# Optimization experiments

Hardware: AMD Instinct MI355X
Metric: run time of the kernel (lower is better)

Reference implementation:

```python
import jax, jax.numpy as jnp
from jax import lax
import numpy as np

B, S_DEC, S_ENC = 32, 128, 128
V, E, H = 32000, 200, 128


def setup_inputs() -> dict:
    key = jax.random.key(0)
    ks = jax.random.split(key, 10)
    emb = jax.random.normal(ks[0], (V, E), dtype=jnp.float32)
    emb = emb.at[0].set(0.0)  # padding_idx row (char2id[' '] -> 0)
    return {
        "sequence": jax.random.randint(ks[1], (B, S_DEC), 0, V),
        "hs": jax.random.normal(ks[2], (B, S_ENC, H), dtype=jnp.float32),
        "h": jax.random.normal(ks[3], (1, B, H), dtype=jnp.float32),
        "emb": emb,
        "w_ih": jax.random.normal(ks[4], (3 * H, E), dtype=jnp.float32) * 0.05,
        "w_hh": jax.random.normal(ks[5], (3 * H, H), dtype=jnp.float32) * 0.05,
        "b_ih": jax.random.normal(ks[6], (3 * H,), dtype=jnp.float32) * 0.05,
        "b_hh": jax.random.normal(ks[7], (3 * H,), dtype=jnp.float32) * 0.05,
        "w_out": jax.random.normal(ks[8], (V, 2 * H), dtype=jnp.float32) * 0.05,
        "b_out": jax.random.normal(ks[9], (V,), dtype=jnp.float32) * 0.05,
    }


def _gru(x_gates, h0, w_hh, b_hh):
    # x_gates: [B, S, 3H] precomputed input projections; torch gate order r,z,n
    def step(hprev, xg):
        hg = hprev @ w_hh.T + b_hh
        xr, xz, xn = jnp.split(xg, 3, axis=-1)
        hr, hz, hn = jnp.split(hg, 3, axis=-1)
        r = jax.nn.sigmoid(xr + hr)
        z = jax.nn.sigmoid(xz + hz)
        n = jnp.tanh(xn + r * hn)
        hnew = (1.0 - z) * n + z * hprev
        return hnew, hnew

    hT, outs = lax.scan(step, h0, jnp.swapaxes(x_gates, 0, 1))  # scan over time
    return jnp.swapaxes(outs, 0, 1), hT  # [B,S,H], [B,H]


def reference(sequence, hs, h, emb, w_ih, w_hh, b_ih, b_hh, w_out, b_out):
    # Embedding lookup (padding row already zero)
    x = emb[sequence]  # [B, S_dec, E]
    x_gates = jnp.einsum("bse,ge->bsg", x, w_ih) + b_ih  # [B, S_dec, 3H]
    output, hT = _gru(x_gates, h[0], w_hh, b_hh)  # [B, S_dec, H]
    state = hT[None]  # [1, B, H]
    # s = bmm(hs, output^T): [B, S_enc, S_dec]; softmax over encoder axis (dim=1)
    s = jnp.einsum("beh,bdh->bed", hs, output)
    attention_weight = jax.nn.softmax(s, axis=1)
    # context: replaces the per-timestep python loop with one contraction
    c = jnp.einsum("bed,beh->bdh", attention_weight, hs)  # [B, S_dec, H]
    cat = jnp.concatenate([output, c], axis=-1)  # [B, S_dec, 2H]
    logits = jnp.einsum("bdh,vh->bdv", cat, w_out) + b_out  # [B, S_dec, V]
    return logits, state, attention_weight
```

## Files before the change

### kernel.cpp

```cpp
#include <hip/hip_runtime.h>
#include <hip/hip_bf16.h>

#define B_    32
#define SDEC  128
#define SENC  128
#define V_    32000
#define E_    200
#define H_    128
#define G3    384

typedef __attribute__((ext_vector_type(8))) short bf16x8;
typedef __attribute__((ext_vector_type(4))) float f32x4;

#define GLOBAL_AS __attribute__((address_space(1)))
#define LDS_AS    __attribute__((address_space(3)))

__device__ __forceinline__ float fast_sigmoid(float x) {
  return 1.f / (1.f + __expf(-x));
}
__device__ __forceinline__ float fast_tanh(float x) {
  float e2 = __expf(2.f * x);
  return 1.f - 2.f / (e2 + 1.f);
}

__global__ __launch_bounds__(192) void k_embed_proj(
    const int* __restrict__ seq, const float* __restrict__ emb,
    const float* __restrict__ w_ih, const float* __restrict__ b_ih,
    float* __restrict__ xg) {
  __shared__ __align__(16) float xs[16][E_];
  __shared__ int sidx[16];
  const int r0 = blockIdx.x * 16;
  const int t = threadIdx.x;
  if (t < 16) sidx[t] = seq[r0 + t];
  __syncthreads();
  for (int i = t; i < 800; i += 192) {
    int r = i / 50, c = i - r * 50;
    *(float4*)&xs[r][c * 4] =
        *(const float4*)(emb + (size_t)sidx[r] * E_ + c * 4);
  }
  __syncthreads();
  const int g0 = t, g1 = t + 192;
  float a0[16], a1[16];
#pragma unroll
  for (int r = 0; r < 16; r++) { a0[r] = 0.f; a1[r] = 0.f; }
  const float* w0 = w_ih + (size_t)g0 * E_;
  const float* w1 = w_ih + (size_t)g1 * E_;
  for (int k = 0; k < E_; k += 4) {
    float4 wv0 = *(const float4*)(w0 + k);
    float4 wv1 = *(const float4*)(w1 + k);
#pragma unroll
    for (int r = 0; r < 16; r++) {
      float4 xv = *(const float4*)&xs[r][k];
      a0[r] += wv0.x * xv.x + wv0.y * xv.y + wv0.z * xv.z + wv0.w * xv.w;
      a1[r] += wv1.x * xv.x + wv1.y * xv.y + wv1.z * xv.z + wv1.w * xv.w;
    }
  }
  const float b0 = b_ih[g0], b1 = b_ih[g1];
#pragma unroll
  for (int r = 0; r < 16; r++) {
    xg[(size_t)(r0 + r) * G3 + g0] = a0[r] + b0;
    xg[(size_t)(r0 + r) * G3 + g1] = a1[r] + b1;
  }
}

__global__ __launch_bounds__(512) void k_gru_cvt(
    const float* __restrict__ xg, const float* __restrict__ h0,
    const float* __restrict__ w_hh, const float* __restrict__ b_hh,
    float* __restrict__ cat, __hip_bfloat16* __restrict__ cat_bf,
    float* __restrict__ state_out,
    const float* __restrict__ w_out, __hip_bfloat16* __restrict__ wout_bf) {
  if (blockIdx.x >= 32) {
    int idx = ((blockIdx.x - 32) * 512 + threadIdx.x) * 8;
    float4 a = *(const float4*)(w_out + idx);
    float4 c = *(const float4*)(w_out + idx + 4);
    union { __hip_bfloat16 h[8]; uint4 v; } p;
    p.h[0] = __float2bfloat16(a.x); p.h[1] = __float2bfloat16(a.y);
    p.h[2] = __float2bfloat16(a.z); p.h[3] = __float2bfloat16(a.w);
    p.h[4] = __float2bfloat16(c.x); p.h[5] = __float2bfloat16(c.y);
    p.h[6] = __float2bfloat16(c.z); p.h[7] = __float2bfloat16(c.w);
    *(uint4*)(wout_bf + idx) = p.v;
    return;
  }

  const int b = blockIdx.x;
  const int t = threadIdx.x;
  const int hh = t >> 2;
  const int sub = t & 3;

  float wr_[32], wz_[32], wn_[32];
#pragma unroll
  for (int m = 0; m < 8; m++) {
    int c = (m + sub * 2) & 7;
    int kb = sub * 32 + c * 4;
    *(float4*)&wr_[m * 4] = *(const float4*)(w_hh + (size_t)hh * H_ + kb);
    *(float4*)&wz_[m * 4] = *(const float4*)(w_hh + (size_t)(128 + hh) * H_ + kb);
    *(float4*)&wn_[m * 4] = *(const float4*)(w_hh + (size_t)(256 + hh) * H_ + kb);
  }

  __shared__ __align__(16) float hp[2][H_];
  const float* xgb = xg + (size_t)b * SDEC * G3;
  const float br = b_hh[hh], bz = b_hh[128 + hh], bn = b_hh[256 + hh];
  float cxr = xgb[hh], cxz = xgb[128 + hh], cxn = xgb[256 + hh];
  if (t < H_) hp[0][t] = h0[b * H_ + t];
  float* catb = cat + (size_t)b * SDEC * 256;
  __hip_bfloat16* catbfb = cat_bf + (size_t)b * SDEC * 256;
  __syncthreads();

  int cur = 0;
  for (int s = 0; s < SDEC; s++) {
    float nxr = 0.f, nxz = 0.f, nxn = 0.f;
    if (s + 1 < SDEC) {
      const float* xp = xgb + (size_t)(s + 1) * G3;
      nxr = xp[hh]; nxz = xp[128 + hh]; nxn = xp[256 + hh];
    }
    float sr = 0.f, sz = 0.f, sn = 0.f;
#pragma unroll
    for (int m = 0; m < 8; m++) {
      int c = (m + sub * 2) & 7;
      float4 hv = *(const float4*)&hp[cur][sub * 32 + c * 4];
      sr += wr_[m * 4 + 0] * hv.x + wr_[m * 4 + 1] * hv.y +
            wr_[m * 4 + 2] * hv.z + wr_[m * 4 + 3] * hv.w;
      sz += wz_[m * 4 + 0] * hv.x + wz_[m * 4 + 1] * hv.y +
            wz_[m * 4 + 2] * hv.z + wz_[m * 4 + 3] * hv.w;
      sn += wn_[m * 4 + 0] * hv.x + wn_[m * 4 + 1] * hv.y +
            wn_[m * 4 + 2] * hv.z + wn_[m * 4 + 3] * hv.w;
    }
    sr += __shfl_xor(sr, 1); sr += __shfl_xor(sr, 2);
    sz += __shfl_xor(sz, 1); sz += __shfl_xor(sz, 2);
    sn += __shfl_xor(sn, 1); sn += __shfl_xor(sn, 2);

    float hold = hp[cur][hh];
    float r = fast_sigmoid(cxr + sr + br);
    float z = fast_sigmoid(cxz + sz + bz);
    float n = fast_tanh(cxn + r * (sn + bn));
    float hnew = (1.f - z) * n + z * hold;
    if (sub == 0) {
      hp[cur ^ 1][hh] = hnew;
      catb[(size_t)s * 256 + hh] = hnew;
      catbfb[(size_t)s * 256 + hh] = __float2bfloat16(hnew);
    }
    __syncthreads();
    cur ^= 1;
    cxr = nxr; cxz = nxz; cxn = nxn;
  }
  if (t < H_) state_out[b * H_ + t] = hp[cur][t];
}

__global__ __launch_bounds__(256) void k_attn(
    const float* __restrict__ hs, const float* __restrict__ cat,
    float* __restrict__ attw_out, __hip_bfloat16* __restrict__ cat_bf) {
  __shared__ __align__(16) float hsb[SENC][H_];
  __shared__ __align__(16) float ctb[64][H_];
  __shared__ __align__(16) float sbuf[64][SENC];
  const int b = blockIdx.x >> 1;
  const int d0 = (blockIdx.x & 1) * 64;
  const int t = threadIdx.x;
  const float* hsbase = hs + (size_t)b * SENC * H_;

  for (int i = t; i < 4096; i += 256) {
    int r = i >> 5, c4 = i & 31;
    int pc = c4 ^ ((r >> 3) & 3);
    *(f32x4*)&hsb[r][pc * 4] = *(const f32x4*)(hsbase + r * H_ + c4 * 4);
  }
  for (int i = t; i < 2048; i += 256) {
    int r = i >> 5, c4 = i & 31;
    int pc = c4 ^ ((r >> 2) & 7);
    *(f32x4*)&ctb[r][pc * 4] =
        *(const f32x4*)(cat + (size_t)(b * SDEC + d0 + r) * 256 + c4 * 4);
  }
  __syncthreads();

  {
    const int te = t >> 4, td = t & 15;
    const int sa = te & 3, sb2 = td & 7;
    float acc[8][4] = {};
    for (int k4 = 0; k4 < 32; k4++) {
      const int pa = (k4 ^ sa) * 4, pb = (k4 ^ sb2) * 4;
      f32x4 av[8], bv[4];
#pragma unroll
      for (int i = 0; i < 8; i++) av[i] = *(const f32x4*)&hsb[te * 8 + i][pa];
#pragma unroll
      for (int j = 0; j < 4; j++) bv[j] = *(const f32x4*)&ctb[td * 4 + j][pb];
#pragma unroll
      for (int i = 0; i < 8; i++)
#pragma unroll
        for (int j = 0; j < 4; j++)
          acc[i][j] += av[i][0] * bv[j][0] + av[i][1] * bv[j][1] +
                       av[i][2] * bv[j][2] + av[i][3] * bv[j][3];
    }
    const int swd = td & 7;
#pragma unroll
    for (int j = 0; j < 4; j++) {
      int drow = td * 4 + j;
      f32x4 v0 = {acc[0][j], acc[1][j], acc[2][j], acc[3][j]};
      f32x4 v1 = {acc[4][j], acc[5][j], acc[6][j], acc[7][j]};
      *(f32x4*)&sbuf[drow][((te * 2) ^ swd) * 4] = v0;
      *(f32x4*)&sbuf[drow][((te * 2 + 1) ^ swd) * 4] = v1;
    }
  }
  __syncthreads();

  {
    const int d = t >> 2, p = t & 3;
    const int swz = (d >> 2) & 7;
    f32x4 vals[8];
    float mx = -1e30f;
#pragma unroll
    for (int mm = 0; mm < 8; mm++) {
      int pc = p * 8 + mm;
      f32x4 v = *(const f32x4*)&sbuf[d][pc * 4];
      vals[mm] = v;
      mx = fmaxf(mx, fmaxf(fmaxf(v[0], v[1]), fmaxf(v[2], v[3])));
    }
    mx = fmaxf(mx, __shfl_xor(mx, 1));
    mx = fmaxf(mx, __shfl_xor(mx, 2));
    float sum = 0.f;
#pragma unroll
    for (int mm = 0; mm < 8; mm++) {
      f32x4 v = vals[mm];
      v[0] = __expf(v[0] - mx); v[1] = __expf(v[1] - mx);
      v[2] = __expf(v[2] - mx); v[3] = __expf(v[3] - mx);
      vals[mm] = v;
      sum += v[0] + v[1] + v[2] + v[3];
    }
    sum += __shfl_xor(sum, 1); sum += __shfl_xor(sum, 2);
    const float inv = 1.f / sum;
    float* aw = attw_out + (size_t)b * SENC * SDEC + d0 + d;
#pragma unroll
    for (int mm = 0; mm < 8; mm++) {
      int pc = p * 8 + mm;
      f32x4 v = vals[mm];
      v[0] *= inv; v[1] *= inv; v[2] *= inv; v[3] *= inv;
      *(f32x4*)&sbuf[d][pc * 4] = v;
      int c4 = pc ^ swz;
#pragma unroll
      for (int u = 0; u < 4; u++)
        aw[(size_t)(c4 * 4 + u) * SDEC] = v[u];
    }
  }
  __syncthreads();

  {
    const int td = t >> 4, th = t & 15;
    const int swd = td & 7;
    float acc[4][8] = {};
    for (int e4 = 0; e4 < 32; e4++) {
      const int pp = (e4 ^ swd) * 4;
      f32x4 pv[4];
#pragma unroll
      for (int i = 0; i < 4; i++) pv[i] = *(const f32x4*)&sbuf[td * 4 + i][pp];
#pragma unroll
      for (int j = 0; j < 4; j++) {
        int e = e4 * 4 + j;
        int sw = (e >> 3) & 3;
        f32x4 h0v = *(const f32x4*)&hsb[e][((th * 2) ^ sw) * 4];
        f32x4 h1v = *(const f32x4*)&hsb[e][((th * 2 + 1) ^ sw) * 4];
#pragma unroll
        for (int i = 0; i < 4; i++) {
          float pw = pv[i][j];
          acc[i][0] += pw * h0v[0]; acc[i][1] += pw * h0v[1];
          acc[i][2] += pw * h0v[2]; acc[i][3] += pw * h0v[3];
          acc[i][4] += pw * h1v[0]; acc[i][5] += pw * h1v[1];
          acc[i][6] += pw * h1v[2]; acc[i][7] += pw * h1v[3];
        }
      }
    }
#pragma unroll
    for (int i = 0; i < 4; i++) {
      union { __hip_bfloat16 hv[8]; uint4 v; } pk;
#pragma unroll
      for (int u = 0; u < 8; u++) pk.hv[u] = __float2bfloat16(acc[i][u]);
      *(uint4*)(cat_bf + (size_t)(b * SDEC + d0 + td * 4 + i) * 256 + 128 +
                th * 8) = pk.v;
    }
  }
}

__global__ __launch_bounds__(512) void k_gemm_mfma(
    const __hip_bfloat16* __restrict__ A, const __hip_bfloat16* __restrict__ Bw,
    const float* __restrict__ b_out, float* __restrict__ C) {
  constexpr int K = 256, N = V_, Kt = 32;
  alignas(16) __shared__ char smem[73728];
  __hip_bfloat16 (*As)[4096] = (__hip_bfloat16(*)[4096])smem;
  __hip_bfloat16 (*Bs)[8192] = (__hip_bfloat16(*)[8192])(smem + 24576);
  float* tr = (float*)smem;

  const int tid = threadIdx.x;
  const int w = tid >> 6, l = tid & 63;
  const int wr = w >> 2, wc = w & 3;
  const int lr = l & 15, lk = l >> 4;
  const int lq = l >> 2, lc = l & 3;

  const int bid = blockIdx.x;
  const int wgid = (bid & 7) * 500 + (bid >> 3);
  const int mt = wgid & 31;
  const int nt = wgid >> 5;
  const int m0 = mt * 128, n0 = nt * 256;

  f32x4 acc[4][4];
#pragma unroll
  for (int m = 0; m < 4; m++)
#pragma unroll
    for (int n = 0; n < 4; n++) acc[m][n] = (f32x4){0.f, 0.f, 0.f, 0.f};

#define STAGE(buf, kk)                                                            \
  do {                                                                            \
    const __hip_bfloat16* gA = A + (size_t)(m0 + w * 16 + lq) * K + (kk) + lc * 8;\
    const __hip_bfloat16* gB0 = Bw + (size_t)(n0 + w * 32 + lq) * K + (kk) + lc * 8;\
    const __hip_bfloat16* gB1 = gB0 + (size_t)16 * K;                             \
    __builtin_amdgcn_global_load_lds((const GLOBAL_AS void*)gA,                   \
        (LDS_AS void*)(&As[buf][w * 512]), 16, 0, 0);                             \
    __builtin_amdgcn_global_load_lds((const GLOBAL_AS void*)gB0,                  \
        (LDS_AS void*)(&Bs[buf][w * 1024]), 16, 0, 0);                            \
    __builtin_amdgcn_global_load_lds((const GLOBAL_AS void*)gB1,                  \
        (LDS_AS void*)(&Bs[buf][w * 1024 + 512]), 16, 0, 0);                      \
  } while (0)

  STAGE(0, 0);
  STAGE(1, Kt);

#pragma unroll
  for (int t = 0; t < 8; ++t) {
    if (t < 7) asm volatile("s_waitcnt vmcnt(3)" ::: "memory");
    else       asm volatile("s_waitcnt vmcnt(0)" ::: "memory");
    __builtin_amdgcn_s_barrier();
    asm volatile("" ::: "memory");

    const int c = t % 3;
    bf16x8 af[4], bfr[4];
#pragma unroll
    for (int m = 0; m < 4; m++)
      af[m] = *(const bf16x8*)(const void*)(&As[c][(wr * 64 + m * 16 + lr) * Kt + lk * 8]);
#pragma unroll
    for (int n = 0; n < 4; n++)
      bfr[n] = *(const bf16x8*)(const void*)(&Bs[c][(wc * 64 + n * 16 + lr) * Kt + lk * 8]);

    if (t < 6) STAGE((t + 2) % 3, (t + 2) * Kt);

#pragma unroll
    for (int m = 0; m < 4; m++)
#pragma unroll
      for (int n = 0; n < 4; n++)
        acc[m][n] = __builtin_amdgcn_mfma_f32_16x16x32_bf16(bfr[n], af[m], acc[m][n], 0, 0, 0);
  }
#undef STAGE

  __syncthreads();
#pragma unroll
  for (int h = 0; h < 2; ++h) {
    if (wr == h) {
#pragma unroll
      for (int m = 0; m < 4; m++) {
#pragma unroll
        for (int n = 0; n < 4; n++) {
          const int row = m * 16 + lr;
          const int col = wc * 64 + n * 16 + lk * 4;
          const float4 bo = *(const float4*)(b_out + n0 + col);
          f32x4 v;
          v[0] = acc[m][n][0] + bo.x;
          v[1] = acc[m][n][1] + bo.y;
          v[2] = acc[m][n][2] + bo.z;
          v[3] = acc[m][n][3] + bo.w;
          *(f32x4*)&tr[row * 260 + col] = v;
        }
      }
    }
    __syncthreads();
#pragma unroll
    for (int i = 0; i < 8; ++i) {
      const int c2 = i * 512 + tid;
      const int row = c2 >> 6;
      const int off = (c2 & 63) * 4;
      f32x4 v = *(const f32x4*)&tr[row * 260 + off];
      __builtin_nontemporal_store(
          v, (f32x4*)(C + (size_t)(m0 + h * 64 + row) * N + n0 + off));
    }
    __syncthreads();
  }
}

extern "C" void kernel_launch(void* const* d_in, const int* in_sizes, int n_in,
                              void* d_out, int out_size, void* d_ws, size_t ws_size,
                              hipStream_t stream) {
  const int* seq = (const int*)d_in[0];
  const float* hs = (const float*)d_in[1];
  const float* h0 = (const float*)d_in[2];
  const float* emb = (const float*)d_in[3];
  const float* w_ih = (const float*)d_in[4];
  const float* w_hh = (const float*)d_in[5];
  const float* b_ih = (const float*)d_in[6];
  const float* b_hh = (const float*)d_in[7];
  const float* w_out = (const float*)d_in[8];
  const float* b_out = (const float*)d_in[9];

  float* out = (float*)d_out;
  float* logits = out;
  float* state = out + 131072000;
  float* attw = out + 131072000 + 4096;

  char* ws = (char*)d_ws;
  float* xg = (float*)ws;
  float* cat = (float*)(ws + 6291456);
  __hip_bfloat16* cat_bf = (__hip_bfloat16*)(ws + 10485760);
  __hip_bfloat16* wout_bf = (__hip_bfloat16*)(ws + 12582912);

  k_embed_proj<<<256, 192, 0, stream>>>(seq, emb, w_ih, b_ih, xg);
  k_gru_cvt<<<2032, 512, 0, stream>>>(xg, h0, w_hh, b_hh, cat, cat_bf, state,
                                      w_out, wout_bf);
  k_attn<<<64, 256, 0, stream>>>(hs, cat, attw, cat_bf);
  k_gemm_mfma<<<4000, 512, 0, stream>>>(cat_bf, wout_bf, b_out, logits);
}
```

Measured before the change: 273.4 us.

## Rewrite attention with bf16 MFMA and drop fp32 GRU output buffer

Replaces the fp32 scalar-FMA attention kernel with one block per batch that runs both score and context matmuls on bf16 MFMA, using swizzled LDS tiles and an in-LDS transpose of hs. The GRU no longer writes the fp32 output copy, and the attention reads the bf16 hidden states instead. The GRU recurrent dot product is rewritten with two-wide float vectors to encourage packed FMA. In exchange, attention scores are computed from bf16 inputs, which lowers precision of the attention weights output, and the attention grid halves to 32 blocks.

```diff
diff --git a/kernel.cpp b/kernel.cpp
--- a/kernel.cpp
+++ b/kernel.cpp
@@ -11,6 +11,7 @@
 
 typedef __attribute__((ext_vector_type(8))) short bf16x8;
 typedef __attribute__((ext_vector_type(4))) float f32x4;
+typedef __attribute__((ext_vector_type(2))) float f32x2;
 
 #define GLOBAL_AS __attribute__((address_space(1)))
 #define LDS_AS    __attribute__((address_space(3)))
@@ -66,8 +67,7 @@
 __global__ __launch_bounds__(512) void k_gru_cvt(
     const float* __restrict__ xg, const float* __restrict__ h0,
     const float* __restrict__ w_hh, const float* __restrict__ b_hh,
-    float* __restrict__ cat, __hip_bfloat16* __restrict__ cat_bf,
-    float* __restrict__ state_out,
+    __hip_bfloat16* __restrict__ cat_bf, float* __restrict__ state_out,
     const float* __restrict__ w_out, __hip_bfloat16* __restrict__ wout_bf) {
   if (blockIdx.x >= 32) {
     int idx = ((blockIdx.x - 32) * 512 + threadIdx.x) * 8;
@@ -102,7 +102,6 @@
   const float br = b_hh[hh], bz = b_hh[128 + hh], bn = b_hh[256 + hh];
   float cxr = xgb[hh], cxz = xgb[128 + hh], cxn = xgb[256 + hh];
   if (t < H_) hp[0][t] = h0[b * H_ + t];
-  float* catb = cat + (size_t)b * SDEC * 256;
   __hip_bfloat16* catbfb = cat_bf + (size_t)b * SDEC * 256;
   __syncthreads();
 
@@ -113,18 +112,22 @@
       const float* xp = xgb + (size_t)(s + 1) * G3;
       nxr = xp[hh]; nxz = xp[128 + hh]; nxn = xp[256 + hh];
     }
-    float sr = 0.f, sz = 0.f, sn = 0.f;
+    f32x2 sr2 = {0.f, 0.f}, sz2 = {0.f, 0.f}, sn2 = {0.f, 0.f};
 #pragma unroll
     for (int m = 0; m < 8; m++) {
       int c = (m + sub * 2) & 7;
       float4 hv = *(const float4*)&hp[cur][sub * 32 + c * 4];
-      sr += wr_[m * 4 + 0] * hv.x + wr_[m * 4 + 1] * hv.y +
-            wr_[m * 4 + 2] * hv.z + wr_[m * 4 + 3] * hv.w;
-      sz += wz_[m * 4 + 0] * hv.x + wz_[m * 4 + 1] * hv.y +
-            wz_[m * 4 + 2] * hv.z + wz_[m * 4 + 3] * hv.w;
-      sn += wn_[m * 4 + 0] * hv.x + wn_[m * 4 + 1] * hv.y +
-            wn_[m * 4 + 2] * hv.z + wn_[m * 4 + 3] * hv.w;
-    }
+      f32x2 h01 = {hv.x, hv.y}, h23 = {hv.z, hv.w};
+      const f32x2* w2r = (const f32x2*)&wr_[m * 4];
+      const f32x2* w2z = (const f32x2*)&wz_[m * 4];
+      const f32x2* w2n = (const f32x2*)&wn_[m * 4];
+      sr2 += w2r[0] * h01; sr2 += w2r[1] * h23;
+      sz2 += w2z[0] * h01; sz2 += w2z[1] * h23;
+      sn2 += w2n[0] * h01; sn2 += w2n[1] * h23;
+    }
+    float sr = sr2[0] + sr2[1];
+    float sz = sz2[0] + sz2[1];
+    float sn = sn2[0] + sn2[1];
     sr += __shfl_xor(sr, 1); sr += __shfl_xor(sr, 2);
     sz += __shfl_xor(sz, 1); sz += __shfl_xor(sz, 2);
     sn += __shfl_xor(sn, 1); sn += __shfl_xor(sn, 2);
@@ -136,7 +139,6 @@
     float hnew = (1.f - z) * n + z * hold;
     if (sub == 0) {
       hp[cur ^ 1][hh] = hnew;
-      catb[(size_t)s * 256 + hh] = hnew;
       catbfb[(size_t)s * 256 + hh] = __float2bfloat16(hnew);
     }
     __syncthreads();
@@ -146,133 +148,129 @@
   if (t < H_) state_out[b * H_ + t] = hp[cur][t];
 }
 
-__global__ __launch_bounds__(256) void k_attn(
-    const float* __restrict__ hs, const float* __restrict__ cat,
-    float* __restrict__ attw_out, __hip_bfloat16* __restrict__ cat_bf) {
-  __shared__ __align__(16) float hsb[SENC][H_];
-  __shared__ __align__(16) float ctb[64][H_];
-  __shared__ __align__(16) float sbuf[64][SENC];
-  const int b = blockIdx.x >> 1;
-  const int d0 = (blockIdx.x & 1) * 64;
+__global__ __launch_bounds__(512) void k_attn_mfma(
+    const float* __restrict__ hs, __hip_bfloat16* __restrict__ cat_bf,
+    float* __restrict__ attw_out) {
+  __shared__ __hip_bfloat16 hsb[128][128];
+  __shared__ __hip_bfloat16 hsT[128][128];
+  __shared__ __hip_bfloat16 ctb[128][128];
+  __shared__ __hip_bfloat16 plds[128][128];
+  const int b = blockIdx.x;
   const int t = threadIdx.x;
+  const int w = t >> 6, l = t & 63;
+  const int lr = l & 15, lk = l >> 4;
   const float* hsbase = hs + (size_t)b * SENC * H_;
 
-  for (int i = t; i < 4096; i += 256) {
-    int r = i >> 5, c4 = i & 31;
-    int pc = c4 ^ ((r >> 3) & 3);
-    *(f32x4*)&hsb[r][pc * 4] = *(const f32x4*)(hsbase + r * H_ + c4 * 4);
-  }
-  for (int i = t; i < 2048; i += 256) {
-    int r = i >> 5, c4 = i & 31;
-    int pc = c4 ^ ((r >> 2) & 7);
-    *(f32x4*)&ctb[r][pc * 4] =
-        *(const f32x4*)(cat + (size_t)(b * SDEC + d0 + r) * 256 + c4 * 4);
-  }
-  __syncthreads();
-
-  {
-    const int te = t >> 4, td = t & 15;
-    const int sa = te & 3, sb2 = td & 7;
-    float acc[8][4] = {};
-    for (int k4 = 0; k4 < 32; k4++) {
-      const int pa = (k4 ^ sa) * 4, pb = (k4 ^ sb2) * 4;
-      f32x4 av[8], bv[4];
-#pragma unroll
-      for (int i = 0; i < 8; i++) av[i] = *(const f32x4*)&hsb[te * 8 + i][pa];
-#pragma unroll
-      for (int j = 0; j < 4; j++) bv[j] = *(const f32x4*)&ctb[td * 4 + j][pb];
-#pragma unroll
-      for (int i = 0; i < 8; i++)
-#pragma unroll
-        for (int j = 0; j < 4; j++)
-          acc[i][j] += av[i][0] * bv[j][0] + av[i][1] * bv[j][1] +
-                       av[i][2] * bv[j][2] + av[i][3] * bv[j][3];
-    }
-    const int swd = td & 7;
-#pragma unroll
-    for (int j = 0; j < 4; j++) {
-      int drow = td * 4 + j;
-      f32x4 v0 = {acc[0][j], acc[1][j], acc[2][j], acc[3][j]};
-      f32x4 v1 = {acc[4][j], acc[5][j], acc[6][j], acc[7][j]};
-      *(f32x4*)&sbuf[drow][((te * 2) ^ swd) * 4] = v0;
-      *(f32x4*)&sbuf[drow][((te * 2 + 1) ^ swd) * 4] = v1;
-    }
-  }
-  __syncthreads();
-
-  {
-    const int d = t >> 2, p = t & 3;
-    const int swz = (d >> 2) & 7;
-    f32x4 vals[8];
-    float mx = -1e30f;
-#pragma unroll
-    for (int mm = 0; mm < 8; mm++) {
-      int pc = p * 8 + mm;
-      f32x4 v = *(const f32x4*)&sbuf[d][pc * 4];
-      vals[mm] = v;
-      mx = fmaxf(mx, fmaxf(fmaxf(v[0], v[1]), fmaxf(v[2], v[3])));
-    }
-    mx = fmaxf(mx, __shfl_xor(mx, 1));
-    mx = fmaxf(mx, __shfl_xor(mx, 2));
-    float sum = 0.f;
-#pragma unroll
-    for (int mm = 0; mm < 8; mm++) {
-      f32x4 v = vals[mm];
-      v[0] = __expf(v[0] - mx); v[1] = __expf(v[1] - mx);
-      v[2] = __expf(v[2] - mx); v[3] = __expf(v[3] - mx);
-      vals[mm] = v;
-      sum += v[0] + v[1] + v[2] + v[3];
-    }
-    sum += __shfl_xor(sum, 1); sum += __shfl_xor(sum, 2);
-    const float inv = 1.f / sum;
-    float* aw = attw_out + (size_t)b * SENC * SDEC + d0 + d;
-#pragma unroll
-    for (int mm = 0; mm < 8; mm++) {
-      int pc = p * 8 + mm;
-      f32x4 v = vals[mm];
-      v[0] *= inv; v[1] *= inv; v[2] *= inv; v[3] *= inv;
-      *(f32x4*)&sbuf[d][pc * 4] = v;
-      int c4 = pc ^ swz;
-#pragma unroll
-      for (int u = 0; u < 4; u++)
-        aw[(size_t)(c4 * 4 + u) * SDEC] = v[u];
-    }
-  }
-  __syncthreads();
-
-  {
-    const int td = t >> 4, th = t & 15;
-    const int swd = td & 7;
-    float acc[4][8] = {};
-    for (int e4 = 0; e4 < 32; e4++) {
-      const int pp = (e4 ^ swd) * 4;
-      f32x4 pv[4];
-#pragma unroll
-      for (int i = 0; i < 4; i++) pv[i] = *(const f32x4*)&sbuf[td * 4 + i][pp];
-#pragma unroll
-      for (int j = 0; j < 4; j++) {
-        int e = e4 * 4 + j;
-        int sw = (e >> 3) & 3;
-        f32x4 h0v = *(const f32x4*)&hsb[e][((th * 2) ^ sw) * 4];
-        f32x4 h1v = *(const f32x4*)&hsb[e][((th * 2 + 1) ^ sw) * 4];
-#pragma unroll
-        for (int i = 0; i < 4; i++) {
-          float pw = pv[i][j];
-          acc[i][0] += pw * h0v[0]; acc[i][1] += pw * h0v[1];
-          acc[i][2] += pw * h0v[2]; acc[i][3] += pw * h0v[3];
-          acc[i][4] += pw * h1v[0]; acc[i][5] += pw * h1v[1];
-          acc[i][6] += pw * h1v[2]; acc[i][7] += pw * h1v[3];
-        }
-      }
-    }
-#pragma unroll
-    for (int i = 0; i < 4; i++) {
-      union { __hip_bfloat16 hv[8]; uint4 v; } pk;
-#pragma unroll
-      for (int u = 0; u < 8; u++) pk.hv[u] = __float2bfloat16(acc[i][u]);
-      *(uint4*)(cat_bf + (size_t)(b * SDEC + d0 + td * 4 + i) * 256 + 128 +
-                th * 8) = pk.v;
-    }
+  for (int i = t; i < 2048; i += 512) {
+    int d = i >> 4, c = i & 15;
+    uint4 v = *(const uint4*)(cat_bf + (size_t)(b * SDEC + d) * 256 + c * 8);
+    *(uint4*)&ctb[d][((c ^ (d & 7)) * 8)] = v;
+  }
+  for (int i = t; i < 2048; i += 512) {
+    int e = i >> 4, c = i & 15;
+    float4 v0 = *(const float4*)(hsbase + e * H_ + c * 8);
+    float4 v1 = *(const float4*)(hsbase + e * H_ + c * 8 + 4);
+    union { __hip_bfloat16 h[8]; uint4 u; } pk;
+    pk.h[0] = __float2bfloat16(v0.x); pk.h[1] = __float2bfloat16(v0.y);
+    pk.h[2] = __float2bfloat16(v0.z); pk.h[3] = __float2bfloat16(v0.w);
+    pk.h[4] = __float2bfloat16(v1.x); pk.h[5] = __float2bfloat16(v1.y);
+    pk.h[6] = __float2bfloat16(v1.z); pk.h[7] = __float2bfloat16(v1.w);
+    *(uint4*)&hsb[e][((c ^ (e & 7)) * 8)] = pk.u;
+  }
+  __syncthreads();
+
+  for (int i = t; i < 2048; i += 512) {
+    int c = i >> 7, e = i & 127;
+    uint4 v = *(const uint4*)&hsb[e][((c ^ (e & 7)) * 8)];
+    const __hip_bfloat16* hv = (const __hip_bfloat16*)&v;
+#pragma unroll
+    for (int u = 0; u < 8; u++) {
+      int h = c * 8 + u;
+      int col = (e + 8 * (h & 15)) & 127;
+      hsT[h][col] = hv[u];
+    }
+  }
+  __syncthreads();
+
+  f32x4 acc[8];
+#pragma unroll
+  for (int et = 0; et < 8; et++) acc[et] = (f32x4){0.f, 0.f, 0.f, 0.f};
+  bf16x8 afrag[4];
+#pragma unroll
+  for (int kt = 0; kt < 4; kt++)
+    afrag[kt] = *(const bf16x8*)&ctb[w * 16 + lr][(((kt * 4 + lk) ^ (lr & 7)) * 8)];
+#pragma unroll
+  for (int et = 0; et < 8; et++) {
+#pragma unroll
+    for (int kt = 0; kt < 4; kt++) {
+      bf16x8 bfrag =
+          *(const bf16x8*)&hsb[et * 16 + lr][(((kt * 4 + lk) ^ (lr & 7)) * 8)];
+      acc[et] =
+          __builtin_amdgcn_mfma_f32_16x16x32_bf16(bfrag, afrag[kt], acc[et], 0, 0, 0);
+    }
+  }
+
+  float mx = -1e30f;
+#pragma unroll
+  for (int et = 0; et < 8; et++) {
+    mx = fmaxf(mx, fmaxf(fmaxf(acc[et][0], acc[et][1]),
+                         fmaxf(acc[et][2], acc[et][3])));
+  }
+  mx = fmaxf(mx, __shfl_xor(mx, 16));
+  mx = fmaxf(mx, __shfl_xor(mx, 32));
+  float sum = 0.f;
+#pragma unroll
+  for (int et = 0; et < 8; et++) {
+    acc[et][0] = __expf(acc[et][0] - mx);
+    acc[et][1] = __expf(acc[et][1] - mx);
+    acc[et][2] = __expf(acc[et][2] - mx);
+    acc[et][3] = __expf(acc[et][3] - mx);
+    sum += acc[et][0] + acc[et][1] + acc[et][2] + acc[et][3];
+  }
+  sum += __shfl_xor(sum, 16);
+  sum += __shfl_xor(sum, 32);
+  const float inv = 1.f / sum;
+
+  const int d = w * 16 + lr;
+  float* aw = attw_out + (size_t)b * SENC * SDEC + d;
+#pragma unroll
+  for (int et = 0; et < 8; et++) {
+    acc[et][0] *= inv; acc[et][1] *= inv;
+    acc[et][2] *= inv; acc[et][3] *= inv;
+    union { __hip_bfloat16 h[4]; uint2 u; } pk4;
+    pk4.h[0] = __float2bfloat16(acc[et][0]);
+    pk4.h[1] = __float2bfloat16(acc[et][1]);
+    pk4.h[2] = __float2bfloat16(acc[et][2]);
+    pk4.h[3] = __float2bfloat16(acc[et][3]);
+    *(uint2*)&plds[d][(((et * 2 + (lk >> 1)) ^ (lr & 7)) * 8 + 4 * (lk & 1))] =
+        pk4.u;
+    const int e0 = et * 16 + lk * 4;
+#pragma unroll
+    for (int j = 0; j < 4; j++)
+      aw[(size_t)(e0 + j) * SDEC] = acc[et][j];
+  }
+  __syncthreads();
+
+  bf16x8 pfrag[4];
+#pragma unroll
+  for (int f = 0; f < 4; f++)
+    pfrag[f] = *(const bf16x8*)&plds[d][(((f * 4 + lk) ^ (lr & 7)) * 8)];
+#pragma unroll
+  for (int ht = 0; ht < 8; ht++) {
+    f32x4 a2 = (f32x4){0.f, 0.f, 0.f, 0.f};
+#pragma unroll
+    for (int kt = 0; kt < 4; kt++) {
+      bf16x8 hfrag =
+          *(const bf16x8*)&hsT[ht * 16 + lr][((kt * 32 + lk * 8 + 8 * lr) & 127)];
+      a2 = __builtin_amdgcn_mfma_f32_16x16x32_bf16(hfrag, pfrag[kt], a2, 0, 0, 0);
+    }
+    union { __hip_bfloat16 h[4]; uint2 u; } pk4;
+    pk4.h[0] = __float2bfloat16(a2[0]);
+    pk4.h[1] = __float2bfloat16(a2[1]);
+    pk4.h[2] = __float2bfloat16(a2[2]);
+    pk4.h[3] = __float2bfloat16(a2[3]);
+    *(uint2*)(cat_bf + (size_t)(b * SDEC + d) * 256 + 128 + ht * 16 + lk * 4) =
+        pk4.u;
   }
 }
 
@@ -400,13 +398,12 @@
 
   char* ws = (char*)d_ws;
   float* xg = (float*)ws;
-  float* cat = (float*)(ws + 6291456);
   __hip_bfloat16* cat_bf = (__hip_bfloat16*)(ws + 10485760);
   __hip_bfloat16* wout_bf = (__hip_bfloat16*)(ws + 12582912);
 
   k_embed_proj<<<256, 192, 0, stream>>>(seq, emb, w_ih, b_ih, xg);
-  k_gru_cvt<<<2032, 512, 0, stream>>>(xg, h0, w_hh, b_hh, cat, cat_bf, state,
+  k_gru_cvt<<<2032, 512, 0, stream>>>(xg, h0, w_hh, b_hh, cat_bf, state,
                                       w_out, wout_bf);
-  k_attn<<<64, 256, 0, stream>>>(hs, cat, attw, cat_bf);
+  k_attn_mfma<<<32, 512, 0, stream>>>(hs, cat_bf, attw);
   k_gemm_mfma<<<4000, 512, 0, stream>>>(cat_bf, wout_bf, b_out, logits);
 }
```

New measurement: 252.2 us. -7.7%, faster.
